# Performance work log

Measured on AMD Instinct MI355X. Metric: run time of the kernel, lower is better.

The kernel has to match this reference:

```python
import jax, jax.numpy as jnp
import numpy as np

N_USERS = 60000
N_ITEMS = 30000
N_NODES = N_USERS + N_ITEMS
D = 64
L = 2


def _norm_adj(edge_index):
    # symmetrize: A_idx = [e, e.flip(0)]
    src = jnp.concatenate([edge_index[0], edge_index[1]])
    dst = jnp.concatenate([edge_index[1], edge_index[0]])
    ones = jnp.ones_like(src, dtype=jnp.float32)
    deg = jax.ops.segment_sum(ones, src, num_segments=N_NODES)
    deg = jnp.clip(deg, 1.0, None)
    val = jax.lax.rsqrt(deg[src]) * jax.lax.rsqrt(deg[dst])
    return src, dst, val


def _spmm(src, dst, val, x):
    # out[i] = sum_{(i,j) in E} val_ij * x[j]
    return jax.ops.segment_sum(val[:, None] * x[dst], src, num_segments=N_NODES)


def setup_inputs() -> dict:
    key = jax.random.key(0)
    ks = jax.random.split(key, 20)
    s = 0.02
    inp = {
        'x_txt': jax.random.normal(ks[0], (N_ITEMS, 768), jnp.float32),
        'x_img': jax.random.normal(ks[1], (N_ITEMS, 512), jnp.float32),
        'x_struct': jax.random.normal(ks[2], (N_ITEMS, 128), jnp.float32),
        'user_emb': jax.random.normal(ks[3], (3, N_USERS, D), jnp.float32) * s,
        'W_txt': jax.random.normal(ks[4], (3, 768, D), jnp.float32) * s,
        'b_txt': jax.random.normal(ks[5], (3, D), jnp.float32) * s,
        'W_img': jax.random.normal(ks[6], (3, 512, D), jnp.float32) * s,
        'b_img': jax.random.normal(ks[7], (3, D), jnp.float32) * s,
        'W_st': jax.random.normal(ks[8], (3, 128, D), jnp.float32) * s,
        'b_st': jax.random.normal(ks[9], (3, D), jnp.float32) * s,
        'Wu1': jax.random.normal(ks[10], (3 * D, 128), jnp.float32) * s,
        'bu1': jax.random.normal(ks[11], (128,), jnp.float32) * s,
        'Wu2': jax.random.normal(ks[12], (128, 3), jnp.float32) * s,
        'bu2': jax.random.normal(ks[13], (3,), jnp.float32) * s,
        'Wi1': jax.random.normal(ks[14], (3 * D, 128), jnp.float32) * s,
        'bi1': jax.random.normal(ks[15], (128,), jnp.float32) * s,
        'Wi2': jax.random.normal(ks[16], (128, 3), jnp.float32) * s,
        'bi2': jax.random.normal(ks[17], (3,), jnp.float32) * s,
        'edge_index': jax.random.randint(ks[18], (2, 500000), 0, N_NODES, jnp.int64),
    }
    return inp


def reference(x_txt, x_img, x_struct, user_emb, W_txt, b_txt, W_img, b_img,
              W_st, b_st, Wu1, bu1, Wu2, bu2, Wi1, bi1, Wi2, bi2, edge_index):
    src, dst, val = _norm_adj(edge_index)

    # item embeddings for all 3 branches at once: [n_items, 3, d]
    i0 = (jnp.einsum('nt,btd->nbd', x_txt, W_txt) + b_txt
          + jnp.einsum('nt,btd->nbd', x_img, W_img) + b_img
          + jnp.einsum('nt,btd->nbd', x_struct, W_st) + b_st)
    u0 = jnp.transpose(user_emb, (1, 0, 2))  # [n_users, 3, d]
    x = jnp.concatenate([u0, i0], axis=0).reshape(N_NODES, 3 * D)

    out = x
    for _ in range(L):
        x = _spmm(src, dst, val, x)
        out = out + x
    out = out / (L + 1)

    stack = out.reshape(N_NODES, 3, D)
    U_stack, I_stack = stack[:N_USERS], stack[N_USERS:]
    U_cat = U_stack.reshape(N_USERS, 3 * D)
    I_cat = I_stack.reshape(N_ITEMS, 3 * D)

    a_u = jax.nn.softmax(jax.nn.relu(U_cat @ Wu1 + bu1) @ Wu2 + bu2, axis=-1)
    a_i = jax.nn.softmax(jax.nn.relu(I_cat @ Wi1 + bi1) @ Wi2 + bi2, axis=-1)

    U = jnp.einsum('nb,nbd->nd', a_u, U_stack)
    I = jnp.einsum('nb,nbd->nd', a_i, I_stack)
    return jnp.concatenate([U, I], axis=0)  # [N_NODES, d]
```

## Files before the change

kernel.cpp:

```cpp
#include <hip/hip_runtime.h>
#include <math.h>

#define N_USERS 60000
#define N_ITEMS 30000
#define N_NODES 90000
#define DD 64
#define FF 192
#define FH 96
#define KK_TOT 1408
#define E_UND 500000
#define E_DIR 1000000
#define SCAN_NBLK 88

typedef __attribute__((ext_vector_type(8))) __bf16 bf16x8;
typedef __attribute__((ext_vector_type(8))) unsigned short u16x8;
typedef __attribute__((ext_vector_type(4))) float f32x4;

typedef __attribute__((address_space(1))) const void gvoid;
typedef __attribute__((address_space(3))) void svoid;

__device__ __forceinline__ void gll16(const void* g, void* l) {
    __builtin_amdgcn_global_load_lds((gvoid*)g, (svoid*)l, 16, 0, 0);
}
__device__ __forceinline__ void fence_bar() {
    asm volatile("" ::: "memory");
    __builtin_amdgcn_s_barrier();
    asm volatile("" ::: "memory");
}

__device__ __forceinline__ unsigned short f2bf(float f) {
    unsigned int u = __float_as_uint(f);
    unsigned int r = (u + 0x7FFFu + ((u >> 16) & 1u)) >> 16;
    return (unsigned short)r;
}
__device__ __forceinline__ float bf_lo(unsigned int x) { return __uint_as_float(x << 16); }
__device__ __forceinline__ float bf_hi(unsigned int x) { return __uint_as_float(x & 0xFFFF0000u); }
__device__ __forceinline__ float bf2f(unsigned short x) {
    return __uint_as_float((unsigned int)x << 16);
}
__device__ __forceinline__ unsigned int pack2(float a, float b) {
    return ((unsigned int)f2bf(b) << 16) | (unsigned int)f2bf(a);
}

__global__ void k_mode(const int* __restrict__ ei, int* __restrict__ mode) {
    __shared__ int any;
    if (threadIdx.x == 0) any = 0;
    __syncthreads();
    if (ei[2 * threadIdx.x + 1] != 0) atomicOr(&any, 1);
    __syncthreads();
    if (threadIdx.x == 0) mode[0] = (any == 0) ? 1 : 0;
}

__device__ __forceinline__ void load_pair(const int* __restrict__ ei, int md, int u,
                                          int& a, int& b) {
    if (md) { a = ei[2 * u]; b = ei[2 * (E_UND + u)]; }
    else    { a = ei[u];     b = ei[E_UND + u]; }
}

__global__ void k_deg(const int* __restrict__ ei, const int* __restrict__ mode,
                      int* __restrict__ deg) {
    int i = blockIdx.x * 256 + threadIdx.x;
    if (i >= E_UND) return;
    int md = mode[0];
    int a, b;
    load_pair(ei, md, i, a, b);
    atomicAdd(&deg[a], 1);
    atomicAdd(&deg[b], 1);
}

__global__ __launch_bounds__(1024) void k_scan1(const int* __restrict__ deg,
                                                int* __restrict__ offs,
                                                int* __restrict__ bsum) {
    __shared__ int tmp[1024];
    int b = blockIdx.x, t = threadIdx.x;
    int i = b * 1024 + t;
    int v = (i < N_NODES) ? deg[i] : 0;
    tmp[t] = v;
    __syncthreads();
    for (int off = 1; off < 1024; off <<= 1) {
        int add = (t >= off) ? tmp[t - off] : 0;
        __syncthreads();
        tmp[t] += add;
        __syncthreads();
    }
    offs[i] = tmp[t] - v;
    if (t == 1023) bsum[b] = tmp[t];
}

__global__ void k_scan2(const int* __restrict__ bsum, int* __restrict__ bscan) {
    if (threadIdx.x == 0) {
        int run = 0;
        for (int b = 0; b < SCAN_NBLK; b++) { bscan[b] = run; run += bsum[b]; }
    }
}

__global__ void k_scan3(const int* __restrict__ deg, int* __restrict__ offs,
                        const int* __restrict__ bscan, int* __restrict__ cursor,
                        float* __restrict__ rsq) {
    int i = blockIdx.x * 256 + threadIdx.x;
    if (i >= N_NODES) return;
    int o = offs[i] + bscan[i >> 10];
    offs[i] = o;
    cursor[i] = o;
    int dg = deg[i];
    if (dg < 1) dg = 1;
    rsq[i] = rsqrtf((float)dg);
}

__global__ void k_fill(const int* __restrict__ ei, const int* __restrict__ mode,
                       int* __restrict__ cursor, const float* __restrict__ rsq,
                       int* __restrict__ edst, float* __restrict__ eval) {
    int i = blockIdx.x * 256 + threadIdx.x;
    if (i >= E_DIR) return;
    int md = mode[0];
    int u = (i < E_UND) ? i : i - E_UND;
    int a, b;
    load_pair(ei, md, u, a, b);
    int s, d;
    if (i < E_UND) { s = a; d = b; } else { s = b; d = a; }
    int slot = atomicAdd(&cursor[s], 1);
    edst[slot] = d;
    eval[slot] = rsq[s] * rsq[d];
}

__global__ void k_users(const float* __restrict__ ue, unsigned short* __restrict__ Xbs) {
    int idx = blockIdx.x * 256 + threadIdx.x;
    if (idx >= N_USERS * FF) return;
    int n = idx / FF;
    int r = idx - n * FF;
    int b = r >> 6, d = r & 63;
    Xbs[idx] = f2bf(ue[((size_t)b * N_USERS + n) * DD + d]);
}

__global__ void k_cvt_w(const float* __restrict__ Wt, const float* __restrict__ Wi,
                        const float* __restrict__ Wst, unsigned short* __restrict__ Wtb) {
    int idx = blockIdx.x * 256 + threadIdx.x;
    if (idx >= FF * KK_TOT) return;
    int n = idx / KK_TOT;
    int k = idx - n * KK_TOT;
    int b = n >> 6, d = n & 63;
    float v;
    if (k < 768)       v = Wt [((size_t)b * 768 + k) * 64 + d];
    else if (k < 1280) v = Wi [((size_t)b * 512 + (k - 768)) * 64 + d];
    else               v = Wst[((size_t)b * 128 + (k - 1280)) * 64 + d];
    Wtb[idx] = f2bf(v);
}

__global__ void k_cvt_w1(const float* __restrict__ Wu1, const float* __restrict__ Wi1,
                         unsigned short* __restrict__ W1Tu,
                         unsigned short* __restrict__ W1Ti) {
    int idx = blockIdx.x * 256 + threadIdx.x;
    if (idx >= 128 * FF) return;
    int n = idx / FF;
    int k = idx - n * FF;
    W1Tu[idx] = f2bf(Wu1[(size_t)k * 128 + n]);
    W1Ti[idx] = f2bf(Wi1[(size_t)k * 128 + n]);
}

#define BM 64
#define BK 64
#define NT (KK_TOT / BK)

__global__ __launch_bounds__(512, 4) void k_item_gemm_mfma3(
    const float* __restrict__ xt, const float* __restrict__ xi, const float* __restrict__ xs,
    const unsigned short* __restrict__ Wtb,
    const float* __restrict__ bt, const float* __restrict__ bi, const float* __restrict__ bst,
    unsigned short* __restrict__ Xbs) {
    __shared__ float          Ashf[2][BM * BK];
    __shared__ unsigned short Bsh [2][FF * BK];
    const int tid  = threadIdx.x;
    const int w    = tid >> 6;
    const int lane = tid & 63;
    const int row0 = blockIdx.x * BM;
    const int l16  = lane & 15;
    const int quad = lane >> 4;
    const int rg   = w & 3;
    const int ng   = w >> 2;

    const int ac = lane & 15;
    const int bc = lane & 7;

    auto stage = [&](int k0, int buf) {
#pragma unroll
        for (int i = 0; i < 2; i++) {
            int rb = w * 8 + i * 4;
            int r  = rb + (lane >> 4);
            int gr = row0 + r; if (gr >= N_ITEMS) gr = N_ITEMS - 1;
            const float* rp;
            if (k0 < 768)       rp = xt + (size_t)gr * 768 + k0;
            else if (k0 < 1280) rp = xi + (size_t)gr * 512 + (k0 - 768);
            else                rp = xs + (size_t)gr * 128 + (k0 - 1280);
            gll16(rp + ((ac ^ (r & 15)) << 2), &Ashf[buf][rb * BK]);
        }
#pragma unroll
        for (int j = 0; j < 3; j++) {
            int rb = w * 24 + j * 8;
            int r  = rb + (lane >> 3);
            gll16(Wtb + (size_t)r * KK_TOT + k0 + ((bc ^ (r & 7)) << 3),
                  &Bsh[buf][rb * BK]);
        }
    };

    f32x4 acc[6];
#pragma unroll
    for (int tn = 0; tn < 6; tn++) acc[tn] = (f32x4){0.f, 0.f, 0.f, 0.f};

    auto compute = [&](int buf) {
#pragma unroll
        for (int kk = 0; kk < BK; kk += 32) {
            const int rA = rg * 16 + l16;
            const float* Ab = &Ashf[buf][rA * BK];
            const int c0 = (kk >> 2) + quad * 2;
            float4 a0 = *(const float4*)(Ab + (((c0    ) ^ l16) << 2));
            float4 a1 = *(const float4*)(Ab + (((c0 + 1) ^ l16) << 2));
            bf16x8 af;
            af[0] = (__bf16)a0.x; af[1] = (__bf16)a0.y;
            af[2] = (__bf16)a0.z; af[3] = (__bf16)a0.w;
            af[4] = (__bf16)a1.x; af[5] = (__bf16)a1.y;
            af[6] = (__bf16)a1.z; af[7] = (__bf16)a1.w;
            const int cB = (kk >> 3) + quad;
#pragma unroll
            for (int tn = 0; tn < 6; tn++) {
                int R = ng * 96 + tn * 16 + l16;
                bf16x8 bfrag = *(const bf16x8*)(&Bsh[buf][R * BK + ((cB ^ (R & 7)) << 3)]);
                acc[tn] = __builtin_amdgcn_mfma_f32_16x16x32_bf16(af, bfrag, acc[tn], 0, 0, 0);
            }
        }
    };

    stage(0, 0);
    int cur = 0;
#pragma unroll 1
    for (int t = 0; t < NT - 1; ++t) {
        fence_bar();
        stage((t + 1) * BK, cur ^ 1);
        asm volatile("s_waitcnt vmcnt(5)" ::: "memory");
        fence_bar();
        compute(cur);
        cur ^= 1;
    }
    fence_bar();
    asm volatile("s_waitcnt vmcnt(0)" ::: "memory");
    fence_bar();
    compute(cur);

#pragma unroll
    for (int tn = 0; tn < 6; tn++) {
        int n = ng * 96 + tn * 16 + l16;
        int b = n >> 6, d = n & 63;
        float bias = bt[b * 64 + d] + bi[b * 64 + d] + bst[b * 64 + d];
#pragma unroll
        for (int r = 0; r < 4; r++) {
            int row = row0 + rg * 16 + quad * 4 + r;
            if (row < N_ITEMS) {
                Xbs[(size_t)(N_USERS + row) * FF + n] = f2bf(acc[tn][r] + bias);
            }
        }
    }
}

__global__ __launch_bounds__(192) void k_spmm_bf(const unsigned int* __restrict__ Xb,
                                                 unsigned int* __restrict__ Yb,
                                                 const int* __restrict__ offs,
                                                 const int* __restrict__ deg,
                                                 const int* __restrict__ edst,
                                                 const float* __restrict__ eval) {
    int t = threadIdx.x;
    int half = (t >= FH) ? 1 : 0;
    int c = t - half * FH;
    int n = blockIdx.x * 2 + half;
    int start = offs[n];
    int dg = deg[n];
    const int* ed = edst + start;
    const float* ev = eval + start;
    float a0 = 0.f, a1 = 0.f;
    for (int j = 0; j < dg; j += 4) {
        int last = dg - 1;
        int j1 = (j + 1 < dg) ? j + 1 : last;
        int j2 = (j + 2 < dg) ? j + 2 : last;
        int j3 = (j + 3 < dg) ? j + 3 : last;
        int d0 = ed[j], d1 = ed[j1], d2 = ed[j2], d3 = ed[j3];
        float v0 = ev[j];
        float v1 = (j + 1 < dg) ? ev[j1] : 0.f;
        float v2 = (j + 2 < dg) ? ev[j2] : 0.f;
        float v3 = (j + 3 < dg) ? ev[j3] : 0.f;
        unsigned int x0 = Xb[(size_t)d0 * FH + c];
        unsigned int x1 = Xb[(size_t)d1 * FH + c];
        unsigned int x2 = Xb[(size_t)d2 * FH + c];
        unsigned int x3 = Xb[(size_t)d3 * FH + c];
        a0 = fmaf(v0, bf_lo(x0), a0); a1 = fmaf(v0, bf_hi(x0), a1);
        a0 = fmaf(v1, bf_lo(x1), a0); a1 = fmaf(v1, bf_hi(x1), a1);
        a0 = fmaf(v2, bf_lo(x2), a0); a1 = fmaf(v2, bf_hi(x2), a1);
        a0 = fmaf(v3, bf_lo(x3), a0); a1 = fmaf(v3, bf_hi(x3), a1);
    }
    Yb[(size_t)n * FH + c] = pack2(a0, a1);
}

#define LDA 200

__global__ __launch_bounds__(256) void k_attn_mfma(
    const unsigned int* __restrict__ X0,
    const unsigned int* __restrict__ X1,
    const unsigned int* __restrict__ X2,
    const unsigned short* __restrict__ W1T,
    const float* __restrict__ B1,
    const float* __restrict__ W2,
    const float* __restrict__ B2,
    float* __restrict__ out,
    int node_base, int n_rows) {
    __shared__ unsigned short Atile[64 * LDA];
    __shared__ float aws[64][4];
    const int tid  = threadIdx.x;
    const int wave = tid >> 6;
    const int lane = tid & 63;
    const int row0 = blockIdx.x * 64;
    const float inv3 = 1.f / 3.f;

#pragma unroll
    for (int i = 0; i < 6; i++) {
        int id = tid + i * 256;
        int r = id / 24;
        int q = id - r * 24;
        u16x8 pk;
        if (row0 + r < n_rows) {
            size_t base = (size_t)(node_base + row0 + r) * FH + q * 4;
            uint4 a = *(const uint4*)(X0 + base);
            uint4 b = *(const uint4*)(X1 + base);
            uint4 c = *(const uint4*)(X2 + base);
            pk[0] = f2bf((bf_lo(a.x) + bf_lo(b.x) + bf_lo(c.x)) * inv3);
            pk[1] = f2bf((bf_hi(a.x) + bf_hi(b.x) + bf_hi(c.x)) * inv3);
            pk[2] = f2bf((bf_lo(a.y) + bf_lo(b.y) + bf_lo(c.y)) * inv3);
            pk[3] = f2bf((bf_hi(a.y) + bf_hi(b.y) + bf_hi(c.y)) * inv3);
            pk[4] = f2bf((bf_lo(a.z) + bf_lo(b.z) + bf_lo(c.z)) * inv3);
            pk[5] = f2bf((bf_hi(a.z) + bf_hi(b.z) + bf_hi(c.z)) * inv3);
            pk[6] = f2bf((bf_lo(a.w) + bf_lo(b.w) + bf_lo(c.w)) * inv3);
            pk[7] = f2bf((bf_hi(a.w) + bf_hi(b.w) + bf_hi(c.w)) * inv3);
        } else {
            pk = (u16x8){0, 0, 0, 0, 0, 0, 0, 0};
        }
        *(u16x8*)(&Atile[r * LDA + q * 8]) = pk;
    }
    __syncthreads();

    f32x4 acc[8];
#pragma unroll
    for (int tn = 0; tn < 8; tn++) acc[tn] = (f32x4){0.f, 0.f, 0.f, 0.f};
    const int l16 = lane & 15;
    const int quad = lane >> 4;
#pragma unroll
    for (int kk = 0; kk < FF; kk += 32) {
        bf16x8 af = *(const bf16x8*)(&Atile[(wave * 16 + l16) * LDA + kk + quad * 8]);
#pragma unroll
        for (int tn = 0; tn < 8; tn++) {
            bf16x8 bf = *(const bf16x8*)(&W1T[(size_t)(tn * 16 + l16) * FF + kk + quad * 8]);
            acc[tn] = __builtin_amdgcn_mfma_f32_16x16x32_bf16(af, bf, acc[tn], 0, 0, 0);
        }
    }

    float pl[4][3];
#pragma unroll
    for (int r = 0; r < 4; r++) { pl[r][0] = 0.f; pl[r][1] = 0.f; pl[r][2] = 0.f; }
#pragma unroll
    for (int tn = 0; tn < 8; tn++) {
        int col = tn * 16 + l16;
        float b1v = B1[col];
        float w0 = W2[col * 3 + 0], w1 = W2[col * 3 + 1], w2v = W2[col * 3 + 2];
#pragma unroll
        for (int r = 0; r < 4; r++) {
            float h = fmaxf(acc[tn][r] + b1v, 0.f);
            pl[r][0] = fmaf(h, w0, pl[r][0]);
            pl[r][1] = fmaf(h, w1, pl[r][1]);
            pl[r][2] = fmaf(h, w2v, pl[r][2]);
        }
    }
#pragma unroll
    for (int m = 1; m <= 8; m <<= 1) {
#pragma unroll
        for (int r = 0; r < 4; r++) {
            pl[r][0] += __shfl_xor(pl[r][0], m, 64);
            pl[r][1] += __shfl_xor(pl[r][1], m, 64);
            pl[r][2] += __shfl_xor(pl[r][2], m, 64);
        }
    }
    float b20 = B2[0], b21 = B2[1], b22 = B2[2];
    if (l16 == 0) {
#pragma unroll
        for (int r = 0; r < 4; r++) {
            float l0 = pl[r][0] + b20, l1 = pl[r][1] + b21, l2 = pl[r][2] + b22;
            float mx = fmaxf(l0, fmaxf(l1, l2));
            float e0 = __expf(l0 - mx), e1 = __expf(l1 - mx), e2 = __expf(l2 - mx);
            float inv = 1.f / (e0 + e1 + e2);
            int rr = wave * 16 + quad * 4 + r;
            aws[rr][0] = e0 * inv; aws[rr][1] = e1 * inv; aws[rr][2] = e2 * inv;
        }
    }
    __syncthreads();

#pragma unroll
    for (int i = 0; i < 16; i++) {
        int flat = tid + i * 256;
        int r = flat >> 6, d = flat & 63;
        if (row0 + r < n_rows) {
            float a0 = aws[r][0], a1 = aws[r][1], a2 = aws[r][2];
            const unsigned short* Ar = &Atile[r * LDA];
            float v = a0 * bf2f(Ar[d]) + a1 * bf2f(Ar[64 + d]) + a2 * bf2f(Ar[128 + d]);
            out[(size_t)(node_base + row0 + r) * DD + d] = v;
        }
    }
}

extern "C" void kernel_launch(void* const* d_in, const int* in_sizes, int n_in,
                              void* d_out, int out_size, void* d_ws, size_t ws_size,
                              hipStream_t stream) {
    (void)in_sizes; (void)n_in; (void)out_size; (void)ws_size;
    const float* x_txt    = (const float*)d_in[0];
    const float* x_img    = (const float*)d_in[1];
    const float* x_struct = (const float*)d_in[2];
    const float* user_emb = (const float*)d_in[3];
    const float* W_txt    = (const float*)d_in[4];
    const float* b_txt    = (const float*)d_in[5];
    const float* W_img    = (const float*)d_in[6];
    const float* b_img    = (const float*)d_in[7];
    const float* W_st     = (const float*)d_in[8];
    const float* b_st     = (const float*)d_in[9];
    const float* Wu1      = (const float*)d_in[10];
    const float* bu1      = (const float*)d_in[11];
    const float* Wu2      = (const float*)d_in[12];
    const float* bu2      = (const float*)d_in[13];
    const float* Wi1      = (const float*)d_in[14];
    const float* bi1      = (const float*)d_in[15];
    const float* Wi2      = (const float*)d_in[16];
    const float* bi2      = (const float*)d_in[17];
    const int*   ei       = (const int*)d_in[18];
    float* out = (float*)d_out;

    char* base = (char*)d_ws;
    size_t off = 0;
    auto take = [&](size_t bytes) -> void* {
        void* p = base + off;
        off += (bytes + 255) & ~(size_t)255;
        return p;
    };
    unsigned int* Xb0  = (unsigned int*)take((size_t)N_NODES * FH * 4);
    unsigned int* Yb   = (unsigned int*)take((size_t)N_NODES * FH * 4);
    unsigned int* Zb   = (unsigned int*)take((size_t)N_NODES * FH * 4);
    int* deg    = (int*)take((size_t)N_NODES * 4);
    int* offs   = (int*)take((size_t)SCAN_NBLK * 1024 * 4);
    int* cursor = (int*)take((size_t)N_NODES * 4);
    int* bsum   = (int*)take((size_t)SCAN_NBLK * 4);
    int* bscan  = (int*)take((size_t)SCAN_NBLK * 4);
    float* rsq  = (float*)take((size_t)N_NODES * 4);
    int* edst   = (int*)take((size_t)E_DIR * 4);
    float* eval = (float*)take((size_t)E_DIR * 4);
    int* mode   = (int*)take(256);
    unsigned short* Wtb  = (unsigned short*)take((size_t)FF * KK_TOT * 2);
    unsigned short* W1Tu = (unsigned short*)take((size_t)128 * FF * 2);
    unsigned short* W1Ti = (unsigned short*)take((size_t)128 * FF * 2);

    hipMemsetAsync(deg, 0, (size_t)N_NODES * 4, stream);

    k_mode<<<1, 256, 0, stream>>>(ei, mode);
    k_deg<<<(E_UND + 255) / 256, 256, 0, stream>>>(ei, mode, deg);
    k_scan1<<<SCAN_NBLK, 1024, 0, stream>>>(deg, offs, bsum);
    k_scan2<<<1, 64, 0, stream>>>(bsum, bscan);
    k_scan3<<<(N_NODES + 255) / 256, 256, 0, stream>>>(deg, offs, bscan, cursor, rsq);
    k_fill<<<(E_DIR + 255) / 256, 256, 0, stream>>>(ei, mode, cursor, rsq, edst, eval);

    k_users<<<(N_USERS * FF + 255) / 256, 256, 0, stream>>>(user_emb,
                                                            (unsigned short*)Xb0);
    k_cvt_w<<<(FF * KK_TOT + 255) / 256, 256, 0, stream>>>(W_txt, W_img, W_st, Wtb);
    k_cvt_w1<<<(128 * FF + 255) / 256, 256, 0, stream>>>(Wu1, Wi1, W1Tu, W1Ti);
    k_item_gemm_mfma3<<<(N_ITEMS + BM - 1) / BM, 512, 0, stream>>>(
        x_txt, x_img, x_struct, Wtb, b_txt, b_img, b_st, (unsigned short*)Xb0);

    k_spmm_bf<<<N_NODES / 2, 192, 0, stream>>>(Xb0, Yb, offs, deg, edst, eval);
    k_spmm_bf<<<N_NODES / 2, 192, 0, stream>>>(Yb, Zb, offs, deg, edst, eval);

    k_attn_mfma<<<(N_USERS + 63) / 64, 256, 0, stream>>>(
        Xb0, Yb, Zb, W1Tu, bu1, Wu2, bu2, out, 0, N_USERS);
    k_attn_mfma<<<(N_ITEMS + 63) / 64, 256, 0, stream>>>(
        Xb0, Yb, Zb, W1Ti, bi1, Wi2, bi2, out, N_USERS, N_ITEMS);
}
```

Before: 604.4 us.

## Drop per-edge weight array and split item GEMM across two column halves

The per-edge normalization array is gone. The SpMM now gathers rsq of each neighbour and scales the row sum by rsq of the destination node. This removes the eval write in the fill kernel and the per-edge eval stream in both SpMM passes, at the cost of a small random gather into a cached table. Separately, the item GEMM moves to 32-row, 96-column tiles with 256-thread blocks, which doubles the block count for more parallelism. The trade-off is that each fp32 activation row is read by two blocks.

Result: slower. 665.6 us (+10.1%).

```diff
diff --git a/kernel.cpp b/kernel.cpp
--- a/kernel.cpp
+++ b/kernel.cpp
@@ -108,8 +108,8 @@
 }
 
 __global__ void k_fill(const int* __restrict__ ei, const int* __restrict__ mode,
-                       int* __restrict__ cursor, const float* __restrict__ rsq,
-                       int* __restrict__ edst, float* __restrict__ eval) {
+                       int* __restrict__ cursor,
+                       int* __restrict__ edst) {
     int i = blockIdx.x * 256 + threadIdx.x;
     if (i >= E_DIR) return;
     int md = mode[0];
@@ -120,7 +120,6 @@
     if (i < E_UND) { s = a; d = b; } else { s = b; d = a; }
     int slot = atomicAdd(&cursor[s], 1);
     edst[slot] = d;
-    eval[slot] = rsq[s] * rsq[d];
 }
 
 __global__ void k_users(const float* __restrict__ ue, unsigned short* __restrict__ Xbs) {
@@ -157,25 +156,27 @@
     W1Ti[idx] = f2bf(Wi1[(size_t)k * 128 + n]);
 }
 
-#define BM 64
+#define BM 32
+#define BNH 96
 #define BK 64
 #define NT (KK_TOT / BK)
 
-__global__ __launch_bounds__(512, 4) void k_item_gemm_mfma3(
+__global__ __launch_bounds__(256, 4) void k_item_gemm_ns(
     const float* __restrict__ xt, const float* __restrict__ xi, const float* __restrict__ xs,
     const unsigned short* __restrict__ Wtb,
     const float* __restrict__ bt, const float* __restrict__ bi, const float* __restrict__ bst,
     unsigned short* __restrict__ Xbs) {
     __shared__ float          Ashf[2][BM * BK];
-    __shared__ unsigned short Bsh [2][FF * BK];
+    __shared__ unsigned short Bsh [2][BNH * BK];
     const int tid  = threadIdx.x;
     const int w    = tid >> 6;
     const int lane = tid & 63;
-    const int row0 = blockIdx.x * BM;
     const int l16  = lane & 15;
     const int quad = lane >> 4;
-    const int rg   = w & 3;
-    const int ng   = w >> 2;
+    const int rg   = w & 1;
+    const int ng   = w >> 1;
+    const int row0 = (blockIdx.x >> 1) * BM;
+    const int n0g  = (blockIdx.x & 1) * BNH;
 
     const int ac = lane & 15;
     const int bc = lane & 7;
@@ -196,14 +197,14 @@
         for (int j = 0; j < 3; j++) {
             int rb = w * 24 + j * 8;
             int r  = rb + (lane >> 3);
-            gll16(Wtb + (size_t)r * KK_TOT + k0 + ((bc ^ (r & 7)) << 3),
+            gll16(Wtb + (size_t)(n0g + r) * KK_TOT + k0 + ((bc ^ (r & 7)) << 3),
                   &Bsh[buf][rb * BK]);
         }
     };
 
-    f32x4 acc[6];
-#pragma unroll
-    for (int tn = 0; tn < 6; tn++) acc[tn] = (f32x4){0.f, 0.f, 0.f, 0.f};
+    f32x4 acc[3];
+#pragma unroll
+    for (int tn = 0; tn < 3; tn++) acc[tn] = (f32x4){0.f, 0.f, 0.f, 0.f};
 
     auto compute = [&](int buf) {
 #pragma unroll
@@ -220,8 +221,8 @@
             af[6] = (__bf16)a1.z; af[7] = (__bf16)a1.w;
             const int cB = (kk >> 3) + quad;
 #pragma unroll
-            for (int tn = 0; tn < 6; tn++) {
-                int R = ng * 96 + tn * 16 + l16;
+            for (int tn = 0; tn < 3; tn++) {
+                int R = ng * 48 + tn * 16 + l16;
                 bf16x8 bfrag = *(const bf16x8*)(&Bsh[buf][R * BK + ((cB ^ (R & 7)) << 3)]);
                 acc[tn] = __builtin_amdgcn_mfma_f32_16x16x32_bf16(af, bfrag, acc[tn], 0, 0, 0);
             }
@@ -245,8 +246,8 @@
     compute(cur);
 
 #pragma unroll
-    for (int tn = 0; tn < 6; tn++) {
-        int n = ng * 96 + tn * 16 + l16;
+    for (int tn = 0; tn < 3; tn++) {
+        int n = n0g + ng * 48 + tn * 16 + l16;
         int b = n >> 6, d = n & 63;
         float bias = bt[b * 64 + d] + bi[b * 64 + d] + bst[b * 64 + d];
 #pragma unroll
@@ -264,7 +265,7 @@
                                                  const int* __restrict__ offs,
                                                  const int* __restrict__ deg,
                                                  const int* __restrict__ edst,
-                                                 const float* __restrict__ eval) {
+                                                 const float* __restrict__ rsq) {
     int t = threadIdx.x;
     int half = (t >= FH) ? 1 : 0;
     int c = t - half * FH;
@@ -272,7 +273,6 @@
     int start = offs[n];
     int dg = deg[n];
     const int* ed = edst + start;
-    const float* ev = eval + start;
     float a0 = 0.f, a1 = 0.f;
     for (int j = 0; j < dg; j += 4) {
         int last = dg - 1;
@@ -280,10 +280,10 @@
         int j2 = (j + 2 < dg) ? j + 2 : last;
         int j3 = (j + 3 < dg) ? j + 3 : last;
         int d0 = ed[j], d1 = ed[j1], d2 = ed[j2], d3 = ed[j3];
-        float v0 = ev[j];
-        float v1 = (j + 1 < dg) ? ev[j1] : 0.f;
-        float v2 = (j + 2 < dg) ? ev[j2] : 0.f;
-        float v3 = (j + 3 < dg) ? ev[j3] : 0.f;
+        float v0 = rsq[d0];
+        float v1 = (j + 1 < dg) ? rsq[d1] : 0.f;
+        float v2 = (j + 2 < dg) ? rsq[d2] : 0.f;
+        float v3 = (j + 3 < dg) ? rsq[d3] : 0.f;
         unsigned int x0 = Xb[(size_t)d0 * FH + c];
         unsigned int x1 = Xb[(size_t)d1 * FH + c];
         unsigned int x2 = Xb[(size_t)d2 * FH + c];
@@ -293,7 +293,8 @@
         a0 = fmaf(v2, bf_lo(x2), a0); a1 = fmaf(v2, bf_hi(x2), a1);
         a0 = fmaf(v3, bf_lo(x3), a0); a1 = fmaf(v3, bf_hi(x3), a1);
     }
-    Yb[(size_t)n * FH + c] = pack2(a0, a1);
+    float rs = rsq[n];
+    Yb[(size_t)n * FH + c] = pack2(a0 * rs, a1 * rs);
 }
 
 #define LDA 200
@@ -451,7 +452,6 @@
     int* bscan  = (int*)take((size_t)SCAN_NBLK * 4);
     float* rsq  = (float*)take((size_t)N_NODES * 4);
     int* edst   = (int*)take((size_t)E_DIR * 4);
-    float* eval = (float*)take((size_t)E_DIR * 4);
     int* mode   = (int*)take(256);
     unsigned short* Wtb  = (unsigned short*)take((size_t)FF * KK_TOT * 2);
     unsigned short* W1Tu = (unsigned short*)take((size_t)128 * FF * 2);
@@ -464,17 +464,17 @@
     k_scan1<<<SCAN_NBLK, 1024, 0, stream>>>(deg, offs, bsum);
     k_scan2<<<1, 64, 0, stream>>>(bsum, bscan);
     k_scan3<<<(N_NODES + 255) / 256, 256, 0, stream>>>(deg, offs, bscan, cursor, rsq);
-    k_fill<<<(E_DIR + 255) / 256, 256, 0, stream>>>(ei, mode, cursor, rsq, edst, eval);
+    k_fill<<<(E_DIR + 255) / 256, 256, 0, stream>>>(ei, mode, cursor, edst);
 
     k_users<<<(N_USERS * FF + 255) / 256, 256, 0, stream>>>(user_emb,
                                                             (unsigned short*)Xb0);
     k_cvt_w<<<(FF * KK_TOT + 255) / 256, 256, 0, stream>>>(W_txt, W_img, W_st, Wtb);
     k_cvt_w1<<<(128 * FF + 255) / 256, 256, 0, stream>>>(Wu1, Wi1, W1Tu, W1Ti);
-    k_item_gemm_mfma3<<<(N_ITEMS + BM - 1) / BM, 512, 0, stream>>>(
+    k_item_gemm_ns<<<((N_ITEMS + BM - 1) / BM) * 2, 256, 0, stream>>>(
         x_txt, x_img, x_struct, Wtb, b_txt, b_img, b_st, (unsigned short*)Xb0);
 
-    k_spmm_bf<<<N_NODES / 2, 192, 0, stream>>>(Xb0, Yb, offs, deg, edst, eval);
-    k_spmm_bf<<<N_NODES / 2, 192, 0, stream>>>(Yb, Zb, offs, deg, edst, eval);
+    k_spmm_bf<<<N_NODES / 2, 192, 0, stream>>>(Xb0, Yb, offs, deg, edst, rsq);
+    k_spmm_bf<<<N_NODES / 2, 192, 0, stream>>>(Yb, Zb, offs, deg, edst, rsq);
 
     k_attn_mfma<<<(N_USERS + 63) / 64, 256, 0, stream>>>(
         Xb0, Yb, Zb, W1Tu, bu1, Wu2, bu2, out, 0, N_USERS);
```
